# Performance work log

Measured on AMD Instinct MI355X. Metric: run time of the kernel, lower is better.

## Reference

```python
import jax, jax.numpy as jnp
import numpy as np
import math

N_LEVELS = 4          # quadtree depth; leaves = 4**4 = 256
N_HEAD = 8
LN_EPS = 1e-5

def _tree_consts():
    # level d has 4**d nodes; offsets[d] = first node index of level d
    sizes = [4 ** d for d in range(N_LEVELS + 1)]
    offsets = np.concatenate([[0], np.cumsum(sizes)])
    n_nodes = int(offsets[-1])  # 341
    parent = np.full(n_nodes, -1, np.int64)
    for d in range(1, N_LEVELS + 1):
        idx = offsets[d] + np.arange(sizes[d])
        parent[idx] = offsets[d - 1] + np.arange(sizes[d]) // 4
    # chain[c, k] = k-th ancestor of c (k=0 -> self); padded by clamping at root
    chain = np.zeros((n_nodes, N_LEVELS + 1), np.int64)
    chain[:, 0] = np.arange(n_nodes)
    for k in range(1, N_LEVELS + 1):
        prev = chain[:, k - 1]
        chain[:, k] = np.where(parent[prev] >= 0, parent[prev], prev)
    nodes_at = [offsets[d] + np.arange(sizes[d]) for d in range(N_LEVELS + 1)]
    return chain, nodes_at, n_nodes

CHAIN, NODES_AT, N_NODES = _tree_consts()

def layernorm(x, g, b):
    m = jnp.mean(x, -1, keepdims=True)
    v = jnp.var(x, -1, keepdims=True)
    return (x - m) * jax.lax.rsqrt(v + LN_EPS) * g + b

def mhsa(x, w_qkv, b_qkv, w_proj, b_proj):
    B, N, E = x.shape
    hd = E // N_HEAD
    qkv = x @ w_qkv + b_qkv                       # (B, N, 3E)
    q, k, v = jnp.split(qkv, 3, axis=-1)
    sh = lambda t: t.reshape(B, N, N_HEAD, hd).transpose(0, 2, 1, 3)  # (B,H,N,hd)
    q, k, v = sh(q), sh(k), sh(v)
    att = jax.nn.softmax(jnp.einsum('bhqd,bhkd->bhqk', q, k) / math.sqrt(hd), axis=-1)
    o = jnp.einsum('bhqk,bhkd->bhqd', att, v).transpose(0, 2, 1, 3).reshape(B, N, E)
    return o @ w_proj + b_proj

def branch_mlp(x, M, b1, w2, b2):
    # Sparse equivalent of einsum('bni,bjmni->bmj', x, W1): W1[:, c, a, :]
    # is nonzero only for a in {c} U ancestors(c), with the weight matrix
    # depending only on (depth(c), depth(a)). Group nodes by depth and sum
    # over ancestor offsets k (depth(a) = d - k).
    B, N, E = x.shape
    h = jnp.zeros((B, N, 4 * E), x.dtype)
    for d in range(N_LEVELS + 1):
        nd = NODES_AT[d]                           # static numpy indices
        acc = jnp.zeros((B, nd.shape[0], 4 * E), x.dtype)
        for k in range(d + 1):
            src = CHAIN[nd, k]                     # ancestor at depth d-k
            acc = acc + jnp.einsum('bne,je->bnj', x[:, src, :], M[d, d - k])
        h = h.at[:, nd, :].set(acc)
    h = jax.nn.relu(h + b1[None, :, :])
    return h @ w2 + b2

def setup_inputs() -> dict:
    key = jax.random.key(0)
    ks = jax.random.split(key, 6)
    B, N, E = 64, N_NODES, 512
    s = 0.02
    return {
        'x': jax.random.normal(ks[0], (B, N, E), jnp.float32),
        'ln1_g': jnp.ones((E,), jnp.float32),
        'ln1_b': jnp.zeros((E,), jnp.float32),
        'w_qkv': jax.random.normal(ks[1], (E, 3 * E), jnp.float32) * s,
        'b_qkv': jnp.zeros((3 * E,), jnp.float32),
        'w_proj': jax.random.normal(ks[2], (E, E), jnp.float32) * s,
        'b_proj': jnp.zeros((E,), jnp.float32),
        'ln2_g': jnp.ones((E,), jnp.float32),
        'ln2_b': jnp.zeros((E,), jnp.float32),
        'mlp_M': jax.random.normal(ks[3], (N_LEVELS + 1, N_LEVELS + 1, 4 * E, E), jnp.float32) * s,
        'mlp_b1': jnp.zeros((N, 4 * E), jnp.float32),
        'w2': jax.random.normal(ks[4], (4 * E, E), jnp.float32) * s,
        'b2': jnp.zeros((E,), jnp.float32),
    }

def reference(x, ln1_g, ln1_b, w_qkv, b_qkv, w_proj, b_proj,
              ln2_g, ln2_b, mlp_M, mlp_b1, w2, b2):
    x = x + mhsa(layernorm(x, ln1_g, ln1_b), w_qkv, b_qkv, w_proj, b_proj)
    x = x + branch_mlp(layernorm(x, ln2_g, ln2_b), mlp_M, mlp_b1, w2, b2)
    return x
```

## Files before the change

kernel.cpp:

```cpp
#include <hip/hip_runtime.h>
#include <hip/hip_bf16.h>


typedef __attribute__((ext_vector_type(8))) __bf16 bf16x8;
typedef __attribute__((ext_vector_type(4))) float f32x4;
typedef __attribute__((ext_vector_type(4))) unsigned int u32x4;

#define GF_RELU    1
#define GF_OUTBF16 2

static __device__ __forceinline__ bf16x8 bzero8() {
    u32x4 z = {0u, 0u, 0u, 0u};
    return __builtin_bit_cast(bf16x8, z);
}

__global__ void transpose_bf16_kernel(const float* __restrict__ in,
                                      __hip_bfloat16* __restrict__ out,
                                      int K, int N, int log2K) {
    int idx = blockIdx.x * 256 + threadIdx.x;
    if (idx >= K * N) return;
    int n = idx >> log2K;
    int k = idx & (K - 1);
    out[idx] = __float2bfloat16(in[(size_t)k * N + n]);
}

__global__ void pack_wcat_kernel(const float* __restrict__ M,
                                 __hip_bfloat16* __restrict__ out) {
    int p = blockIdx.y;
    int s, d;
    if (p < 5)       { s = 0; d = p; }
    else if (p < 9)  { s = 1; d = p - 4; }
    else if (p < 12) { s = 2; d = p - 7; }
    else if (p < 14) { s = 3; d = p - 9; }
    else             { s = 4; d = 4; }
    const int base_lut[5] = {0, 5, 9, 12, 14};
    size_t idx = (size_t)blockIdx.x * 256 + threadIdx.x;
    const size_t MB = 2048ull * 512;
    out[(size_t)base_lut[s] * MB + (size_t)(d - s) * MB + idx] =
        __float2bfloat16(M[((size_t)d * 5 + s) * MB + idx]);
}

__global__ __launch_bounds__(256) void ln_kernel(const float* __restrict__ x,
                                                 const float* __restrict__ g,
                                                 const float* __restrict__ b,
                                                 __hip_bfloat16* __restrict__ out) {
    int tok = blockIdx.x;
    const float* xr = x + (size_t)tok * 512;
    int t = threadIdx.x;
    float v0 = xr[t], v1 = xr[t + 256];
    float s = v0 + v1;
    float s2 = v0 * v0 + v1 * v1;
    #pragma unroll
    for (int o = 32; o > 0; o >>= 1) {
        s  += __shfl_down(s, o);
        s2 += __shfl_down(s2, o);
    }
    __shared__ float ps[4], ps2[4];
    int w = t >> 6, lane = t & 63;
    if (lane == 0) { ps[w] = s; ps2[w] = s2; }
    __syncthreads();
    if (t == 0) {
        float ts = 0.f, ts2 = 0.f;
        #pragma unroll
        for (int i = 0; i < 4; i++) { ts += ps[i]; ts2 += ps2[i]; }
        ps[0] = ts * (1.f / 512.f);
        ps2[0] = ts2 * (1.f / 512.f);
    }
    __syncthreads();
    float m = ps[0];
    float var = ps2[0] - m * m;
    float r = rsqrtf(var + 1e-5f);
    out[(size_t)tok * 512 + t]       = __float2bfloat16((v0 - m) * r * g[t] + b[t]);
    out[(size_t)tok * 512 + t + 256] = __float2bfloat16((v1 - m) * r * g[t + 256] + b[t + 256]);
}

#define ATT_STR 72
__global__ __launch_bounds__(256) void attn_mfma_kernel(const __hip_bfloat16* __restrict__ qkv,
                                                        __hip_bfloat16* __restrict__ ctx) {
    __shared__ __bf16 kt_lds[64 * ATT_STR];
    __shared__ __bf16 vt_lds[64 * ATT_STR];
    __shared__ __bf16 pbuf[4 * 48 * ATT_STR];

    const int bh = blockIdx.x;
    const int half = blockIdx.y;
    const int b = bh >> 3, h = bh & 7;
    const int tid = threadIdx.x;
    const int w = tid >> 6, lane = tid & 63;
    const int q = lane >> 4, l16 = lane & 15;
    const int rowbase = half * 192 + w * 48;
    __bf16* pw = pbuf + w * 48 * ATT_STR;

    bf16x8 qf[3][2];
    #pragma unroll
    for (int mi = 0; mi < 3; mi++) {
        int row = rowbase + mi * 16 + l16;
        #pragma unroll
        for (int ks = 0; ks < 2; ks++) {
            if (row < 341)
                qf[mi][ks] = *(const bf16x8*)(qkv + (size_t)(b * 341 + row) * 1536 +
                                              h * 64 + ks * 32 + q * 8);
            else
                qf[mi][ks] = bzero8();
        }
    }

    f32x4 O[3][4];
    float mrun[3][4], lrun[3][4];
    #pragma unroll
    for (int mi = 0; mi < 3; mi++) {
        #pragma unroll
        for (int ni = 0; ni < 4; ni++) { f32x4 z = {0.f,0.f,0.f,0.f}; O[mi][ni] = z; }
        #pragma unroll
        for (int rr = 0; rr < 4; rr++) { mrun[mi][rr] = -1e30f; lrun[mi][rr] = 0.f; }
    }

    for (int kt6 = 0; kt6 < 6; kt6++) {
        const int kbase = kt6 * 64;
        __syncthreads();
        {
            int key = tid >> 2, kg = tid & 3;
            int gk = kbase + key;
            bf16x8 a0 = bzero8(), a1 = bzero8();
            if (gk < 341) {
                const __hip_bfloat16* src =
                    qkv + (size_t)(b * 341 + gk) * 1536 + 512 + h * 64 + kg * 16;
                a0 = *(const bf16x8*)src;
                a1 = *(const bf16x8*)(src + 8);
            }
            *(bf16x8*)(kt_lds + key * ATT_STR + kg * 16)     = a0;
            *(bf16x8*)(kt_lds + key * ATT_STR + kg * 16 + 8) = a1;
        }
        {
            int key = tid & 63, dg = tid >> 6;
            int gk = kbase + key;
            bf16x8 a0 = bzero8(), a1 = bzero8();
            if (gk < 341) {
                const __hip_bfloat16* src =
                    qkv + (size_t)(b * 341 + gk) * 1536 + 1024 + h * 64 + dg * 16;
                a0 = *(const bf16x8*)src;
                a1 = *(const bf16x8*)(src + 8);
            }
            #pragma unroll
            for (int j = 0; j < 8; j++) {
                vt_lds[(dg * 16 + j) * ATT_STR + key]     = a0[j];
                vt_lds[(dg * 16 + 8 + j) * ATT_STR + key] = a1[j];
            }
        }
        __syncthreads();

        f32x4 S[3][4];
        #pragma unroll
        for (int mi = 0; mi < 3; mi++)
            #pragma unroll
            for (int ni = 0; ni < 4; ni++) { f32x4 z = {0.f,0.f,0.f,0.f}; S[mi][ni] = z; }
        #pragma unroll
        for (int ks = 0; ks < 2; ks++) {
            bf16x8 bf_[4];
            #pragma unroll
            for (int ni = 0; ni < 4; ni++)
                bf_[ni] = *(const bf16x8*)(kt_lds + (ni * 16 + l16) * ATT_STR + ks * 32 + q * 8);
            #pragma unroll
            for (int mi = 0; mi < 3; mi++)
                #pragma unroll
                for (int ni = 0; ni < 4; ni++)
                    S[mi][ni] = __builtin_amdgcn_mfma_f32_16x16x32_bf16(qf[mi][ks], bf_[ni],
                                                                        S[mi][ni], 0, 0, 0);
        }

        float cmask[4];
        #pragma unroll
        for (int ni = 0; ni < 4; ni++)
            cmask[ni] = (kbase + ni * 16 + l16 < 341) ? 0.f : -1e30f;

        #pragma unroll
        for (int mi = 0; mi < 3; mi++) {
            #pragma unroll
            for (int rr = 0; rr < 4; rr++) {
                float rmax = -1e30f;
                #pragma unroll
                for (int ni = 0; ni < 4; ni++)
                    rmax = fmaxf(rmax, fmaf(S[mi][ni][rr], 0.125f, cmask[ni]));
                rmax = fmaxf(rmax, __shfl_xor(rmax, 1));
                rmax = fmaxf(rmax, __shfl_xor(rmax, 2));
                rmax = fmaxf(rmax, __shfl_xor(rmax, 4));
                rmax = fmaxf(rmax, __shfl_xor(rmax, 8));
                float mnew = fmaxf(mrun[mi][rr], rmax);
                float alpha = __expf(mrun[mi][rr] - mnew);
                mrun[mi][rr] = mnew;
                float psum = 0.f;
                #pragma unroll
                for (int ni = 0; ni < 4; ni++) {
                    float p = __expf(fmaf(S[mi][ni][rr], 0.125f, cmask[ni]) - mnew);
                    S[mi][ni][rr] = p;
                    psum += p;
                    O[mi][ni][rr] *= alpha;
                }
                psum += __shfl_xor(psum, 1);
                psum += __shfl_xor(psum, 2);
                psum += __shfl_xor(psum, 4);
                psum += __shfl_xor(psum, 8);
                lrun[mi][rr] = lrun[mi][rr] * alpha + psum;
            }
            #pragma unroll
            for (int ni = 0; ni < 4; ni++)
                #pragma unroll
                for (int rr = 0; rr < 4; rr++)
                    pw[(mi * 16 + q * 4 + rr) * ATT_STR + ni * 16 + l16] =
                        (__bf16)S[mi][ni][rr];
        }
        __syncthreads();

        #pragma unroll
        for (int ks = 0; ks < 2; ks++) {
            bf16x8 pf[3], vf[4];
            #pragma unroll
            for (int mi = 0; mi < 3; mi++)
                pf[mi] = *(const bf16x8*)(pw + (mi * 16 + l16) * ATT_STR + ks * 32 + q * 8);
            #pragma unroll
            for (int ni = 0; ni < 4; ni++)
                vf[ni] = *(const bf16x8*)(vt_lds + (ni * 16 + l16) * ATT_STR + ks * 32 + q * 8);
            #pragma unroll
            for (int mi = 0; mi < 3; mi++)
                #pragma unroll
                for (int ni = 0; ni < 4; ni++)
                    O[mi][ni] = __builtin_amdgcn_mfma_f32_16x16x32_bf16(pf[mi], vf[ni],
                                                                        O[mi][ni], 0, 0, 0);
        }
    }

    #pragma unroll
    for (int mi = 0; mi < 3; mi++) {
        #pragma unroll
        for (int rr = 0; rr < 4; rr++) {
            int row = rowbase + mi * 16 + q * 4 + rr;
            if (row >= 341) continue;
            float inv = 1.f / lrun[mi][rr];
            __hip_bfloat16* op = ctx + (size_t)(b * 341 + row) * 512 + h * 64;
            #pragma unroll
            for (int ni = 0; ni < 4; ni++)
                op[ni * 16 + l16] = __float2bfloat16(O[mi][ni][rr] * inv);
        }
    }
}

static __device__ __forceinline__ int xcd_remap(int bid, int nwg) {
    const int xcd = bid & 7, o = bid >> 3;
    const int qq = nwg >> 3, rr = nwg & 7;
    return (xcd < rr ? xcd * (qq + 1) : rr * (qq + 1) + (xcd - rr) * qq) + o;
}

template <bool GATHER>
static __device__ __forceinline__ void gemm128_body(
    __hip_bfloat16* As, __hip_bfloat16* Bs,
    const __hip_bfloat16* __restrict__ A, const __hip_bfloat16* __restrict__ Bt,
    const float* __restrict__ bias, const float* __restrict__ resid,
    float* __restrict__ Cf, __hip_bfloat16* __restrict__ Cb,
    int Mrows, int N, int K, int flags, int depth, int bm0, int bn0) {
    const int tid = threadIdx.x;
    const int r = tid >> 1;
    const int khalf = tid & 1;
    const int gr = bm0 + r;
    const int gn = bn0 + r;
    const int lane = tid & 63;
    const int w = tid >> 6;
    const int wm = (w >> 1) << 6;
    const int wn = (w & 1) << 6;
    const int q = lane >> 4;
    const int l16 = lane & 15;

    int wsl[4];
    #pragma unroll
    for (int j = 0; j < 4; j++)
        wsl[j] = ((((khalf << 2) | j) ^ (r & 7)) << 3);
    const int rs0 = ((q ^ (l16 & 7)) << 3);
    const int rs1 = (((4 + q) ^ (l16 & 7)) << 3);

    size_t abase;
    if (GATHER) {
        const int dsh = depth << 1;
        const int bmask = (1 << dsh) - 1;
        int b = gr >> dsh;
        int i = gr & bmask;
        int node = (0x55555555 & bmask) + i;
        abase = ((size_t)(b * 341 + node)) << 9;
    } else {
        abase = (size_t)gr * K;
    }

    f32x4 acc[4][4];
    #pragma unroll
    for (int i = 0; i < 4; i++)
        #pragma unroll
        for (int j = 0; j < 4; j++) {
            f32x4 z = {0.f, 0.f, 0.f, 0.f};
            acc[i][j] = z;
        }

    for (int k0 = 0; k0 < K; k0 += 64) {
        bf16x8 va[4], vb[4];
        if (gr < Mrows) {
            const bf16x8* p = (const bf16x8*)(A + abase + k0 + (khalf << 5));
            #pragma unroll
            for (int j = 0; j < 4; j++) va[j] = p[j];
        } else {
            #pragma unroll
            for (int j = 0; j < 4; j++) va[j] = bzero8();
        }
        {
            const bf16x8* p = (const bf16x8*)(Bt + (size_t)gn * K + k0 + (khalf << 5));
            #pragma unroll
            for (int j = 0; j < 4; j++) vb[j] = p[j];
        }
        __syncthreads();
        #pragma unroll
        for (int j = 0; j < 4; j++) {
            *(bf16x8*)(As + r * 64 + wsl[j]) = va[j];
            *(bf16x8*)(Bs + r * 64 + wsl[j]) = vb[j];
        }
        __syncthreads();
        bf16x8 af[4][2], bfr[4][2];
        #pragma unroll
        for (int mi = 0; mi < 4; mi++) {
            const __hip_bfloat16* rp = As + (wm + mi * 16 + l16) * 64;
            af[mi][0] = *(const bf16x8*)(rp + rs0);
            af[mi][1] = *(const bf16x8*)(rp + rs1);
        }
        #pragma unroll
        for (int ni = 0; ni < 4; ni++) {
            const __hip_bfloat16* rp = Bs + (wn + ni * 16 + l16) * 64;
            bfr[ni][0] = *(const bf16x8*)(rp + rs0);
            bfr[ni][1] = *(const bf16x8*)(rp + rs1);
        }
        #pragma unroll
        for (int ks = 0; ks < 2; ks++)
            #pragma unroll
            for (int mi = 0; mi < 4; mi++)
                #pragma unroll
                for (int ni = 0; ni < 4; ni++)
                    acc[mi][ni] = __builtin_amdgcn_mfma_f32_16x16x32_bf16(
                        af[mi][ks], bfr[ni][ks], acc[mi][ni], 0, 0, 0);
    }

    #pragma unroll
    for (int mi = 0; mi < 4; mi++) {
        #pragma unroll
        for (int rr = 0; rr < 4; rr++) {
            int grow = bm0 + wm + mi * 16 + q * 4 + rr;
            if (grow >= Mrows) continue;
            size_t obase = (size_t)grow * N;
            #pragma unroll
            for (int ni = 0; ni < 4; ni++) {
                int col = bn0 + wn + ni * 16 + l16;
                float v = acc[mi][ni][rr];
                if (bias) v += bias[col];
                if (resid) v += resid[obase + col];
                if (flags & GF_RELU) v = fmaxf(v, 0.f);
                if (flags & GF_OUTBF16)
                    Cb[obase + col] = __float2bfloat16(v);
                else
                    Cf[obase + col] = v;
            }
        }
    }
}

__global__ __launch_bounds__(256) void gemm128(
    const __hip_bfloat16* __restrict__ A, const __hip_bfloat16* __restrict__ Bt,
    const float* __restrict__ bias, const float* __restrict__ resid,
    float* __restrict__ Cf, __hip_bfloat16* __restrict__ Cb,
    int Mrows, int N, int K, int flags, int gridN) {
    __shared__ __hip_bfloat16 As[128 * 64];
    __shared__ __hip_bfloat16 Bs[128 * 64];
    const int lin = xcd_remap(blockIdx.x, gridDim.x);
    const int bx = lin / gridN;
    const int by = lin - bx * gridN;
    gemm128_body<false>(As, Bs, A, Bt, bias, resid, Cf, Cb,
                        Mrows, N, K, flags, 0, bx << 7, by << 7);
}

__global__ __launch_bounds__(256, 6) void gemm64(
    const __hip_bfloat16* __restrict__ A, const __hip_bfloat16* __restrict__ Bt,
    const float* __restrict__ bias, const float* __restrict__ resid,
    float* __restrict__ Cf, __hip_bfloat16* __restrict__ Cb,
    int Mrows, int N, int K, int flags, int gridN) {
    __shared__ __hip_bfloat16 As[64 * 64];
    __shared__ __hip_bfloat16 Bs[128 * 64];
    const int lin = xcd_remap(blockIdx.x, gridDim.x);
    const int bx = lin / gridN;
    const int by = lin - bx * gridN;
    const int bm0 = bx << 6, bn0 = by << 7;

    const int tid = threadIdx.x;
    const int ra = tid >> 2, kq = tid & 3;
    const int rb = tid >> 1, khalf = tid & 1;
    const int lane = tid & 63;
    const int w = tid >> 6;
    const int wn = w << 5;
    const int q = lane >> 4;
    const int l16 = lane & 15;

    const int gra = bm0 + ra;
    const int gnb = bn0 + rb;

    int wslA[2];
    #pragma unroll
    for (int j = 0; j < 2; j++)
        wslA[j] = ((((kq << 1) | j) ^ (ra & 7)) << 3);
    int wslB[4];
    #pragma unroll
    for (int j = 0; j < 4; j++)
        wslB[j] = ((((khalf << 2) | j) ^ (rb & 7)) << 3);
    const int rs0 = ((q ^ (l16 & 7)) << 3);
    const int rs1 = (((4 + q) ^ (l16 & 7)) << 3);

    const size_t abase = (size_t)gra * K;

    f32x4 acc[4][2];
    #pragma unroll
    for (int i = 0; i < 4; i++)
        #pragma unroll
        for (int j = 0; j < 2; j++) {
            f32x4 z = {0.f, 0.f, 0.f, 0.f};
            acc[i][j] = z;
        }

    for (int k0 = 0; k0 < K; k0 += 64) {
        bf16x8 va[2], vb[4];
        if (gra < Mrows) {
            const bf16x8* p = (const bf16x8*)(A + abase + k0 + (kq << 4));
            #pragma unroll
            for (int j = 0; j < 2; j++) va[j] = p[j];
        } else {
            #pragma unroll
            for (int j = 0; j < 2; j++) va[j] = bzero8();
        }
        {
            const bf16x8* p = (const bf16x8*)(Bt + (size_t)gnb * K + k0 + (khalf << 5));
            #pragma unroll
            for (int j = 0; j < 4; j++) vb[j] = p[j];
        }
        __syncthreads();
        #pragma unroll
        for (int j = 0; j < 2; j++)
            *(bf16x8*)(As + ra * 64 + wslA[j]) = va[j];
        #pragma unroll
        for (int j = 0; j < 4; j++)
            *(bf16x8*)(Bs + rb * 64 + wslB[j]) = vb[j];
        __syncthreads();
        bf16x8 af[4][2], bfr[2][2];
        #pragma unroll
        for (int mi = 0; mi < 4; mi++) {
            const __hip_bfloat16* rp = As + (mi * 16 + l16) * 64;
            af[mi][0] = *(const bf16x8*)(rp + rs0);
            af[mi][1] = *(const bf16x8*)(rp + rs1);
        }
        #pragma unroll
        for (int ni = 0; ni < 2; ni++) {
            const __hip_bfloat16* rp = Bs + (wn + ni * 16 + l16) * 64;
            bfr[ni][0] = *(const bf16x8*)(rp + rs0);
            bfr[ni][1] = *(const bf16x8*)(rp + rs1);
        }
        #pragma unroll
        for (int ks = 0; ks < 2; ks++)
            #pragma unroll
            for (int mi = 0; mi < 4; mi++)
                #pragma unroll
                for (int ni = 0; ni < 2; ni++)
                    acc[mi][ni] = __builtin_amdgcn_mfma_f32_16x16x32_bf16(
                        af[mi][ks], bfr[ni][ks], acc[mi][ni], 0, 0, 0);
    }

    #pragma unroll
    for (int mi = 0; mi < 4; mi++) {
        #pragma unroll
        for (int rr = 0; rr < 4; rr++) {
            int grow = bm0 + mi * 16 + q * 4 + rr;
            if (grow >= Mrows) continue;
            size_t obase = (size_t)grow * N;
            #pragma unroll
            for (int ni = 0; ni < 2; ni++) {
                int col = bn0 + wn + ni * 16 + l16;
                float v = acc[mi][ni][rr];
                if (bias) v += bias[col];
                if (resid) v += resid[obase + col];
                if (flags & GF_RELU) v = fmaxf(v, 0.f);
                if (flags & GF_OUTBF16)
                    Cb[obase + col] = __float2bfloat16(v);
                else
                    Cf[obase + col] = v;
            }
        }
    }
}

__global__ __launch_bounds__(256) void gemm_branch_fused(
    const __hip_bfloat16* __restrict__ xn, const __hip_bfloat16* __restrict__ wcat,
    __hip_bfloat16* __restrict__ Y) {
    __shared__ __hip_bfloat16 As[128 * 64];
    __shared__ __hip_bfloat16 Bs[128 * 64];
    const int lin = xcd_remap(blockIdx.x, gridDim.x);
    int s;
    if (lin < 80)        s = 0;
    else if (lin < 208)  s = 1;
    else if (lin < 592)  s = 2;
    else if (lin < 1616) s = 3;
    else                 s = 4;
    const int base_tab[5] = {0, 80, 208, 592, 1616};
    const int gn_tab[5]   = {80, 64, 48, 32, 16};
    const size_t yoff[5]  = {0, 655360, 2752512, 9043968, 25821184};
    const int wcat_off[5] = {0, 5, 9, 12, 14};
    const int loc = lin - base_tab[s];
    const int gn = gn_tab[s];
    const int bx = loc / gn;
    const int by = loc - bx * gn;
    const int Mrows = 64 << (s << 1);
    const int N = (5 - s) << 11;
    gemm128_body<true>(As, Bs, xn, wcat + (size_t)wcat_off[s] * (2048ull * 512),
                       nullptr, nullptr, nullptr, Y + yoff[s],
                       Mrows, N, 512, GF_OUTBF16, s, bx << 7, by << 7);
}

__global__ __launch_bounds__(256) void combine_kernel(const __hip_bfloat16* __restrict__ Y,
                                                      const float* __restrict__ b1,
                                                      __hip_bfloat16* __restrict__ h) {
    const size_t yoff[5] = {0, 655360, 2752512, 9043968, 25821184};
    int row = blockIdx.x;
    int b = row / 341;
    int node = row - b * 341;
    int d = (node >= 85) ? 4 : (node >= 21) ? 3 : (node >= 5) ? 2 : (node >= 1) ? 1 : 0;
    int i = node - (0x55555555 & ((1 << (d << 1)) - 1));
    int j = threadIdx.x << 3;

    float acc[8];
    const float* bp = b1 + (size_t)node * 2048 + j;
    f32x4 b0 = *(const f32x4*)bp;
    f32x4 b4 = *(const f32x4*)(bp + 4);
    #pragma unroll
    for (int u = 0; u < 4; u++) { acc[u] = b0[u]; acc[u + 4] = b4[u]; }

    #pragma unroll
    for (int s = 0; s < 5; s++) {
        if (s <= d) {
            int a = i >> ((d - s) << 1);
            int width = (5 - s) << 11;
            const bf16x8 v = *(const bf16x8*)(Y + yoff[s] +
                (size_t)((b << (s << 1)) + a) * width + ((d - s) << 11) + j);
            #pragma unroll
            for (int u = 0; u < 8; u++) acc[u] += (float)v[u];
        }
    }
    bf16x8 o;
    #pragma unroll
    for (int u = 0; u < 8; u++) o[u] = (__bf16)fmaxf(acc[u], 0.f);
    *(bf16x8*)(h + (size_t)row * 2048 + j) = o;
}

extern "C" void kernel_launch(void* const* d_in, const int* in_sizes, int n_in,
                              void* d_out, int out_size, void* d_ws, size_t ws_size,
                              hipStream_t stream) {
    const float* x      = (const float*)d_in[0];
    const float* ln1_g  = (const float*)d_in[1];
    const float* ln1_b  = (const float*)d_in[2];
    const float* w_qkv  = (const float*)d_in[3];
    const float* b_qkv  = (const float*)d_in[4];
    const float* w_proj = (const float*)d_in[5];
    const float* b_proj = (const float*)d_in[6];
    const float* ln2_g  = (const float*)d_in[7];
    const float* ln2_b  = (const float*)d_in[8];
    const float* mlp_M  = (const float*)d_in[9];
    const float* mlp_b1 = (const float*)d_in[10];
    const float* w2     = (const float*)d_in[11];
    const float* b2     = (const float*)d_in[12];
    float* out = (float*)d_out;

    const int M = 64 * 341;

    char* ws = (char*)d_ws;
    size_t off = 0;
    auto alloc = [&](size_t bytes) -> char* {
        char* p = ws + off;
        off += (bytes + 255) & ~(size_t)255;
        return p;
    };
    __hip_bfloat16* xn     = (__hip_bfloat16*)alloc((size_t)M * 512 * 2);
    __hip_bfloat16* wqkvT  = (__hip_bfloat16*)alloc(1536ull * 512 * 2);
    __hip_bfloat16* wprojT = (__hip_bfloat16*)alloc(512ull * 512 * 2);
    __hip_bfloat16* w2T    = (__hip_bfloat16*)alloc(512ull * 2048 * 2);
    __hip_bfloat16* wcat   = (__hip_bfloat16*)alloc(15ull * 2048 * 512 * 2);
    __hip_bfloat16* hbuf   = (__hip_bfloat16*)alloc((size_t)M * 2048 * 2);
    const size_t qkv_bytes = (size_t)M * 1536 * 2;
    const size_t y_bytes   = 59375616ull * 2;
    char* shared = alloc(y_bytes);
    __hip_bfloat16* qkv = (__hip_bfloat16*)shared;
    __hip_bfloat16* ctx = (__hip_bfloat16*)(shared + qkv_bytes);
    __hip_bfloat16* Y   = (__hip_bfloat16*)shared;
    if (off > ws_size) return;

    auto g128 = [&](const __hip_bfloat16* A, const __hip_bfloat16* Bt,
                    const float* bias, const float* resid, float* Cf,
                    __hip_bfloat16* Cb, int Mr, int N, int K, int flags) {
        int gm = (Mr + 127) >> 7, gn = N >> 7;
        gemm128<<<dim3(gm * gn), 256, 0, stream>>>(
            A, Bt, bias, resid, Cf, Cb, Mr, N, K, flags, gn);
    };
    auto g64 = [&](const __hip_bfloat16* A, const __hip_bfloat16* Bt,
                   const float* bias, const float* resid, float* Cf,
                   __hip_bfloat16* Cb, int Mr, int N, int K, int flags) {
        int gm = (Mr + 63) >> 6, gn = N >> 7;
        gemm64<<<dim3(gm * gn), 256, 0, stream>>>(
            A, Bt, bias, resid, Cf, Cb, Mr, N, K, flags, gn);
    };

    transpose_bf16_kernel<<<(512 * 1536 + 255) / 256, 256, 0, stream>>>(w_qkv, wqkvT, 512, 1536, 9);
    transpose_bf16_kernel<<<(512 * 512 + 255) / 256, 256, 0, stream>>>(w_proj, wprojT, 512, 512, 9);
    transpose_bf16_kernel<<<(2048 * 512 + 255) / 256, 256, 0, stream>>>(w2, w2T, 2048, 512, 11);
    pack_wcat_kernel<<<dim3(4096, 15), 256, 0, stream>>>(mlp_M, wcat);

    ln_kernel<<<M, 256, 0, stream>>>(x, ln1_g, ln1_b, xn);
    g128(xn, wqkvT, b_qkv, nullptr, nullptr, qkv, M, 1536, 512, GF_OUTBF16);
    attn_mfma_kernel<<<dim3(512, 2), 256, 0, stream>>>(qkv, ctx);
    g64(ctx, wprojT, b_proj, x, out, nullptr, M, 512, 512, 0);

    ln_kernel<<<M, 256, 0, stream>>>(out, ln2_g, ln2_b, xn);
    gemm_branch_fused<<<dim3(3664), 256, 0, stream>>>(xn, wcat, Y);
    combine_kernel<<<M, 256, 0, stream>>>(Y, mlp_b1, hbuf);
    g64(hbuf, w2T, b2, out, out, nullptr, M, 512, 2048, 0);
}
```

Baseline: 732.0 us.

## Fuse branch combine, bias and ReLU into the w2 GEMM A-tile load

Removes the separate combine kernel and the bf16 hbuf intermediate. The final w2 GEMM now builds its A tile on the fly by summing b1 and the ancestor Y slices for each row, applying ReLU and converting to bf16 before staging into shared memory. This avoids writing and rereading a large M x 2048 activation buffer. In exchange, the GEMM's A loads become gathered and are repeated for each of the 4 N-tiles, and the extra per-row address arithmetic adds register pressure.

```diff
diff --git a/kernel.cpp b/kernel.cpp
--- a/kernel.cpp
+++ b/kernel.cpp
@@ -488,6 +488,155 @@
                     Cb[obase + col] = __float2bfloat16(v);
                 else
                     Cf[obase + col] = v;
+            }
+        }
+    }
+}
+
+__global__ __launch_bounds__(256, 6) void gemm64_w2(
+    const __hip_bfloat16* __restrict__ Y, const float* __restrict__ b1,
+    const __hip_bfloat16* __restrict__ Bt, const float* __restrict__ bias,
+    float* __restrict__ outio, int gridN) {
+    __shared__ __hip_bfloat16 As[64 * 64];
+    __shared__ __hip_bfloat16 Bs[128 * 64];
+    const size_t yoff[5] = {0, 655360, 2752512, 9043968, 25821184};
+    const int Mrows = 21824, N = 512, K = 2048;
+
+    const int lin = xcd_remap(blockIdx.x, gridDim.x);
+    const int bx = lin / gridN;
+    const int by = lin - bx * gridN;
+    const int bm0 = bx << 6, bn0 = by << 7;
+
+    const int tid = threadIdx.x;
+    const int ra = tid >> 2, kq = tid & 3;
+    const int rb = tid >> 1, khalf = tid & 1;
+    const int lane = tid & 63;
+    const int w = tid >> 6;
+    const int wn = w << 5;
+    const int q = lane >> 4;
+    const int l16 = lane & 15;
+
+    const int gnb = bn0 + rb;
+
+    int wslA[2];
+    #pragma unroll
+    for (int j = 0; j < 2; j++)
+        wslA[j] = ((((kq << 1) | j) ^ (ra & 7)) << 3);
+    int wslB[4];
+    #pragma unroll
+    for (int j = 0; j < 4; j++)
+        wslB[j] = ((((khalf << 2) | j) ^ (rb & 7)) << 3);
+    const int rs0 = ((q ^ (l16 & 7)) << 3);
+    const int rs1 = (((4 + q) ^ (l16 & 7)) << 3);
+
+    const int grow = bm0 + ra;
+    const int b = grow / 341;
+    const int node = grow - b * 341;
+    const int d = (node >= 85) ? 4 : (node >= 21) ? 3 : (node >= 5) ? 2
+                 : (node >= 1) ? 1 : 0;
+    const int i = node - (0x55555555 & ((1 << (d << 1)) - 1));
+    size_t ybase[5];
+    #pragma unroll
+    for (int s = 0; s < 5; s++) {
+        if (s <= d) {
+            int ds = d - s;
+            int a = i >> (ds << 1);
+            int rowY = (b << (s << 1)) + a;
+            ybase[s] = yoff[s] + (size_t)rowY * ((5 - s) << 11) + (ds << 11) +
+                       (kq << 4);
+        } else {
+            ybase[s] = 0;
+        }
+    }
+    const float* b1p = b1 + (size_t)node * 2048 + (kq << 4);
+
+    f32x4 acc[4][2];
+    #pragma unroll
+    for (int ii = 0; ii < 4; ii++)
+        #pragma unroll
+        for (int j = 0; j < 2; j++) {
+            f32x4 z = {0.f, 0.f, 0.f, 0.f};
+            acc[ii][j] = z;
+        }
+
+    for (int k0 = 0; k0 < K; k0 += 64) {
+        float av[16];
+        {
+            const f32x4* bp = (const f32x4*)(b1p + k0);
+            #pragma unroll
+            for (int u = 0; u < 4; u++) {
+                f32x4 t = bp[u];
+                av[u * 4 + 0] = t[0]; av[u * 4 + 1] = t[1];
+                av[u * 4 + 2] = t[2]; av[u * 4 + 3] = t[3];
+            }
+        }
+        #pragma unroll
+        for (int s = 0; s < 5; s++) {
+            if (s <= d) {
+                const bf16x8* yp = (const bf16x8*)(Y + ybase[s] + k0);
+                bf16x8 y0 = yp[0], y1 = yp[1];
+                #pragma unroll
+                for (int u = 0; u < 8; u++) {
+                    av[u]     += (float)y0[u];
+                    av[u + 8] += (float)y1[u];
+                }
+            }
+        }
+        bf16x8 va[2];
+        #pragma unroll
+        for (int u = 0; u < 8; u++) {
+            va[0][u] = (__bf16)fmaxf(av[u], 0.f);
+            va[1][u] = (__bf16)fmaxf(av[u + 8], 0.f);
+        }
+        bf16x8 vb[4];
+        {
+            const bf16x8* p = (const bf16x8*)(Bt + (size_t)gnb * K + k0 + (khalf << 5));
+            #pragma unroll
+            for (int j = 0; j < 4; j++) vb[j] = p[j];
+        }
+        __syncthreads();
+        #pragma unroll
+        for (int j = 0; j < 2; j++)
+            *(bf16x8*)(As + ra * 64 + wslA[j]) = va[j];
+        #pragma unroll
+        for (int j = 0; j < 4; j++)
+            *(bf16x8*)(Bs + rb * 64 + wslB[j]) = vb[j];
+        __syncthreads();
+        bf16x8 af[4][2], bfr[2][2];
+        #pragma unroll
+        for (int mi = 0; mi < 4; mi++) {
+            const __hip_bfloat16* rp = As + (mi * 16 + l16) * 64;
+            af[mi][0] = *(const bf16x8*)(rp + rs0);
+            af[mi][1] = *(const bf16x8*)(rp + rs1);
+        }
+        #pragma unroll
+        for (int ni = 0; ni < 2; ni++) {
+            const __hip_bfloat16* rp = Bs + (wn + ni * 16 + l16) * 64;
+            bfr[ni][0] = *(const bf16x8*)(rp + rs0);
+            bfr[ni][1] = *(const bf16x8*)(rp + rs1);
+        }
+        #pragma unroll
+        for (int ks = 0; ks < 2; ks++)
+            #pragma unroll
+            for (int mi = 0; mi < 4; mi++)
+                #pragma unroll
+                for (int ni = 0; ni < 2; ni++)
+                    acc[mi][ni] = __builtin_amdgcn_mfma_f32_16x16x32_bf16(
+                        af[mi][ks], bfr[ni][ks], acc[mi][ni], 0, 0, 0);
+    }
+
+    #pragma unroll
+    for (int mi = 0; mi < 4; mi++) {
+        #pragma unroll
+        for (int rr = 0; rr < 4; rr++) {
+            int growo = bm0 + mi * 16 + q * 4 + rr;
+            if (growo >= Mrows) continue;
+            size_t obase = (size_t)growo * N;
+            #pragma unroll
+            for (int ni = 0; ni < 2; ni++) {
+                int col = bn0 + wn + ni * 16 + l16;
+                float v = acc[mi][ni][rr] + bias[col] + outio[obase + col];
+                outio[obase + col] = v;
             }
         }
     }
@@ -520,41 +669,6 @@
                        Mrows, N, 512, GF_OUTBF16, s, bx << 7, by << 7);
 }
 
-__global__ __launch_bounds__(256) void combine_kernel(const __hip_bfloat16* __restrict__ Y,
-                                                      const float* __restrict__ b1,
-                                                      __hip_bfloat16* __restrict__ h) {
-    const size_t yoff[5] = {0, 655360, 2752512, 9043968, 25821184};
-    int row = blockIdx.x;
-    int b = row / 341;
-    int node = row - b * 341;
-    int d = (node >= 85) ? 4 : (node >= 21) ? 3 : (node >= 5) ? 2 : (node >= 1) ? 1 : 0;
-    int i = node - (0x55555555 & ((1 << (d << 1)) - 1));
-    int j = threadIdx.x << 3;
-
-    float acc[8];
-    const float* bp = b1 + (size_t)node * 2048 + j;
-    f32x4 b0 = *(const f32x4*)bp;
-    f32x4 b4 = *(const f32x4*)(bp + 4);
-    #pragma unroll
-    for (int u = 0; u < 4; u++) { acc[u] = b0[u]; acc[u + 4] = b4[u]; }
-
-    #pragma unroll
-    for (int s = 0; s < 5; s++) {
-        if (s <= d) {
-            int a = i >> ((d - s) << 1);
-            int width = (5 - s) << 11;
-            const bf16x8 v = *(const bf16x8*)(Y + yoff[s] +
-                (size_t)((b << (s << 1)) + a) * width + ((d - s) << 11) + j);
-            #pragma unroll
-            for (int u = 0; u < 8; u++) acc[u] += (float)v[u];
-        }
-    }
-    bf16x8 o;
-    #pragma unroll
-    for (int u = 0; u < 8; u++) o[u] = (__bf16)fmaxf(acc[u], 0.f);
-    *(bf16x8*)(h + (size_t)row * 2048 + j) = o;
-}
-
 extern "C" void kernel_launch(void* const* d_in, const int* in_sizes, int n_in,
                               void* d_out, int out_size, void* d_ws, size_t ws_size,
                               hipStream_t stream) {
@@ -587,7 +701,6 @@
     __hip_bfloat16* wprojT = (__hip_bfloat16*)alloc(512ull * 512 * 2);
     __hip_bfloat16* w2T    = (__hip_bfloat16*)alloc(512ull * 2048 * 2);
     __hip_bfloat16* wcat   = (__hip_bfloat16*)alloc(15ull * 2048 * 512 * 2);
-    __hip_bfloat16* hbuf   = (__hip_bfloat16*)alloc((size_t)M * 2048 * 2);
     const size_t qkv_bytes = (size_t)M * 1536 * 2;
     const size_t y_bytes   = 59375616ull * 2;
     char* shared = alloc(y_bytes);
@@ -623,6 +736,5 @@
 
     ln_kernel<<<M, 256, 0, stream>>>(out, ln2_g, ln2_b, xn);
     gemm_branch_fused<<<dim3(3664), 256, 0, stream>>>(xn, wcat, Y);
-    combine_kernel<<<M, 256, 0, stream>>>(Y, mlp_b1, hbuf);
-    g64(hbuf, w2T, b2, out, out, nullptr, M, 512, 2048, 0);
-}
+    gemm64_w2<<<dim3(1364), 256, 0, stream>>>(Y, mlp_b1, w2T, b2, out, 4);
+}
```

Measured after the change: 776.5 us. 1.06x slower.
